# Performance work log

Hardware: AMD Instinct MI355X
Metric: run time of the kernel (lower is better)

Reference implementation:

```python
import jax, jax.numpy as jnp
import numpy as np

NUM_RAYS = 8192
NUM_POINTS = 1024
NEAR, FAR = 0.1, 6.0


def setup_inputs() -> dict:
    key = jax.random.key(0)
    k_rgb, k_alpha, k_jit, k_dir = jax.random.split(key, 4)
    raw_rgb_per_point = jax.random.uniform(k_rgb, (NUM_RAYS, NUM_POINTS, 3), dtype=jnp.float32)
    raw_alpha = jax.random.normal(k_alpha, (NUM_RAYS, NUM_POINTS), dtype=jnp.float32)
    # Monotonically increasing z values per ray (linspace + stratified jitter)
    t = jnp.linspace(0.0, 1.0, NUM_POINTS)[None, :]  # [1, P]
    jitter = jax.random.uniform(k_jit, (NUM_RAYS, NUM_POINTS), dtype=jnp.float32) / NUM_POINTS
    z_vals = (NEAR + (FAR - NEAR) * jnp.clip(t + jitter, 0.0, 1.0)).astype(jnp.float32)
    z_vals = jnp.sort(z_vals, axis=-1)
    rays_dir = jax.random.normal(k_dir, (NUM_RAYS, 3), dtype=jnp.float32)
    pruning_mask = jnp.ones((NUM_RAYS, NUM_POINTS), dtype=bool)
    return {
        "raw_rgb_per_point": raw_rgb_per_point,
        "raw_alpha": raw_alpha,
        "z_vals": z_vals,
        "rays_dir": rays_dir,
        "pruning_mask": pruning_mask,
        "points_per_ray": NUM_POINTS,
    }


def reference(raw_rgb_per_point, raw_alpha, z_vals, rays_dir, pruning_mask, points_per_ray):
    # Faithful eval-mode (is_training=False) translation of Renderer._compose_rays.
    corrective_factor = float(points_per_ray) / 1024.0
    FAR_DIST = 1e10

    # Distances between adjacent samples, last one padded to "infinity".
    dists = z_vals[..., 1:] - z_vals[..., :-1]                      # [R, P-1]
    dists = jnp.concatenate(
        [dists, jnp.full_like(dists[..., :1], FAR_DIST)], axis=-1)  # [R, P]
    dists = dists * jnp.linalg.norm(rays_dir, axis=-1, keepdims=True)

    # raw2alpha: 1 - exp(-relu(raw) * dist * cf)
    alpha = 1.0 - jnp.exp(-jax.nn.relu(raw_alpha) * dists * corrective_factor)  # [R, P]

    # Exclusive cumulative transmittance, then weights.
    trans = jnp.cumprod(
        jnp.concatenate([jnp.ones_like(alpha[:, :1]), 1.0 - alpha + 1e-10], axis=-1),
        axis=-1)[:, :-1]                                            # [R, P]
    weights = alpha * trans                                         # [R, P]

    rgb = jnp.einsum("rp,rpc->rc", weights, raw_rgb_per_point)      # [R, 3]
    accumulated_weights = jnp.sum(weights, axis=-1)                 # [R]

    depth = (jnp.sum(weights[:, :-1] * z_vals[:, :-1], axis=-1)
             + (1.0 - accumulated_weights + weights[:, -1]) * z_vals[:, -1])  # [R]

    disparity = 1.0 / jnp.maximum(1e-4, depth / accumulated_weights)          # [R]

    return rgb, accumulated_weights, depth, disparity
```

## Files before the change

kernel.cpp:

```cpp
#include <hip/hip_runtime.h>


#define NUM_RAYS 8192
#define P 1024
#define BLOCK 256
#define RAYS_PER_BLOCK 4

__global__ __launch_bounds__(256) void compose_rays_kernel(
    const float* __restrict__ rgb_in,
    const float* __restrict__ raw_alpha,
    const float* __restrict__ z_vals,
    const float* __restrict__ rays_dir,
    const int*   __restrict__ ppr,
    float* __restrict__ out)
{
    const int lane = threadIdx.x & 63;
    const int wid  = threadIdx.x >> 6;
    const int r    = blockIdx.x * RAYS_PER_BLOCK + wid;

    const float cf = (float)(*ppr) * (1.0f / 1024.0f);

    const float dx = rays_dir[r * 3 + 0];
    const float dy = rays_dir[r * 3 + 1];
    const float dz = rays_dir[r * 3 + 2];
    const float nrm = sqrtf(dx * dx + dy * dy + dz * dz);

    const size_t rowP = (size_t)r * P;

    float4 z4[4];
#pragma unroll
    for (int it = 0; it < 4; ++it)
        z4[it] = *(const float4*)(z_vals + rowP + it * 256 + lane * 4);

    float znext[4];
#pragma unroll
    for (int it = 0; it < 4; ++it) {
        const float from_next_lane = __shfl_down(z4[it].x, 1);
        const float first_of_next  = (it < 3) ? __shfl(z4[it + 1].x, 0) : 0.0f;
        znext[it] = (lane == 63) ? first_of_next : from_next_lane;
    }
    const float zl = __shfl(z4[3].w, 63);

    float carry = 1.0f;
    float ws = 0.f, rs = 0.f, gs = 0.f, bs = 0.f, ds = 0.f;
    float wlast = 0.f;

#pragma unroll
    for (int it = 0; it < 4; ++it) {
        const float4 a4 = *(const float4*)(raw_alpha + rowP + it * 256 + lane * 4);
        const float* rgbp = rgb_in + (size_t)r * (P * 3) + it * 768 + lane * 12;
        const float4 c0 = *(const float4*)(rgbp + 0);
        const float4 c1 = *(const float4*)(rgbp + 4);
        const float4 c2 = *(const float4*)(rgbp + 8);

        const float zv[4] = {z4[it].x, z4[it].y, z4[it].z, z4[it].w};
        const float av[4] = {a4.x, a4.y, a4.z, a4.w};
        float dists[4];
        dists[0] = (zv[1] - zv[0]) * nrm;
        dists[1] = (zv[2] - zv[1]) * nrm;
        dists[2] = (zv[3] - zv[2]) * nrm;
        dists[3] = ((it == 3 && lane == 63) ? 1e10f : (znext[it] - zv[3])) * nrm;

        float alpha[4], om[4];
        float local = 1.0f;
#pragma unroll
        for (int j = 0; j < 4; ++j) {
            const float ra = fmaxf(av[j], 0.0f);
            alpha[j] = 1.0f - expf(-ra * dists[j] * cf);
            om[j]    = 1.0f - alpha[j] + 1e-10f;
            local   *= om[j];
        }

        float v = local;
#pragma unroll
        for (int off = 1; off < 64; off <<= 1) {
            const float n = __shfl_up(v, off);
            if (lane >= off) v *= n;
        }
        const float total = __shfl(v, 63);
        float excl = __shfl_up(v, 1);
        if (lane == 0) excl = 1.0f;
        excl *= carry;
        carry *= total;

        const float rgbv[12] = {c0.x, c0.y, c0.z, c0.w, c1.x, c1.y, c1.z, c1.w,
                                c2.x, c2.y, c2.z, c2.w};
        float trun = excl;
#pragma unroll
        for (int j = 0; j < 4; ++j) {
            const float w = alpha[j] * trun;
            ws += w;
            rs += w * rgbv[3 * j + 0];
            gs += w * rgbv[3 * j + 1];
            bs += w * rgbv[3 * j + 2];
            if (it == 3 && lane == 63 && j == 3)
                wlast = w;
            else
                ds += w * zv[j];
            trun *= om[j];
        }
    }

    const float wl = __shfl(wlast, 63);

#pragma unroll
    for (int off = 32; off > 0; off >>= 1) {
        ws += __shfl_down(ws, off);
        rs += __shfl_down(rs, off);
        gs += __shfl_down(gs, off);
        bs += __shfl_down(bs, off);
        ds += __shfl_down(ds, off);
    }

    if (lane == 0) {
        const float depth = ds + (1.0f - ws + wl) * zl;
        const float disp  = 1.0f / fmaxf(1e-4f, depth / ws);
        out[r * 3 + 0] = rs;
        out[r * 3 + 1] = gs;
        out[r * 3 + 2] = bs;
        out[3 * NUM_RAYS + r] = ws;
        out[4 * NUM_RAYS + r] = depth;
        out[5 * NUM_RAYS + r] = disp;
    }
}

extern "C" void kernel_launch(void* const* d_in, const int* in_sizes, int n_in,
                              void* d_out, int out_size, void* d_ws, size_t ws_size,
                              hipStream_t stream) {
    const float* rgb_in    = (const float*)d_in[0];
    const float* raw_alpha = (const float*)d_in[1];
    const float* z_vals    = (const float*)d_in[2];
    const float* rays_dir  = (const float*)d_in[3];
    const int*   ppr       = (const int*)d_in[5];
    float* out = (float*)d_out;

    compose_rays_kernel<<<NUM_RAYS / RAYS_PER_BLOCK, BLOCK, 0, stream>>>(
        rgb_in, raw_alpha, z_vals, rays_dir, ppr, out);
}
```

Before: 31.25 us.

## Coalesce RGB loads and redistribute weights through LDS for colour accumulation

RGB loads change from a 48-byte per-lane stride to fully contiguous float4 loads across the wave. Each lane's four per-point weights are staged in shared memory so lanes can fetch the weights matching their interleaved RGB components. The block shrinks to two rays (128 threads). The change adds LDS traffic, a wait, and per-lane branching on the component phase in exchange for better load coalescing on the dominant RGB stream.

```diff
diff --git a/kernel.cpp b/kernel.cpp
--- a/kernel.cpp
+++ b/kernel.cpp
@@ -3,10 +3,10 @@
 
 #define NUM_RAYS 8192
 #define P 1024
-#define BLOCK 256
-#define RAYS_PER_BLOCK 4
+#define BLOCK 128
+#define RAYS_PER_BLOCK 2
 
-__global__ __launch_bounds__(256) void compose_rays_kernel(
+__global__ __launch_bounds__(128) void compose_rays_kernel(
     const float* __restrict__ rgb_in,
     const float* __restrict__ raw_alpha,
     const float* __restrict__ z_vals,
@@ -17,6 +17,8 @@
     const int lane = threadIdx.x & 63;
     const int wid  = threadIdx.x >> 6;
     const int r    = blockIdx.x * RAYS_PER_BLOCK + wid;
+
+    __shared__ float w_lds[RAYS_PER_BLOCK][4][256];
 
     const float cf = (float)(*ppr) * (1.0f / 1024.0f);
 
@@ -48,10 +50,10 @@
 #pragma unroll
     for (int it = 0; it < 4; ++it) {
         const float4 a4 = *(const float4*)(raw_alpha + rowP + it * 256 + lane * 4);
-        const float* rgbp = rgb_in + (size_t)r * (P * 3) + it * 768 + lane * 12;
-        const float4 c0 = *(const float4*)(rgbp + 0);
-        const float4 c1 = *(const float4*)(rgbp + 4);
-        const float4 c2 = *(const float4*)(rgbp + 8);
+        const float* cbase = rgb_in + (size_t)r * (P * 3) + it * 768;
+        const float4 c0 = *(const float4*)(cbase + 4 * (lane));
+        const float4 c1 = *(const float4*)(cbase + 4 * (lane + 64));
+        const float4 c2 = *(const float4*)(cbase + 4 * (lane + 128));
 
         const float zv[4] = {z4[it].x, z4[it].y, z4[it].z, z4[it].w};
         const float av[4] = {a4.x, a4.y, a4.z, a4.w};
@@ -83,21 +85,44 @@
         excl *= carry;
         carry *= total;
 
-        const float rgbv[12] = {c0.x, c0.y, c0.z, c0.w, c1.x, c1.y, c1.z, c1.w,
-                                c2.x, c2.y, c2.z, c2.w};
-        float trun = excl;
+        float4 wq;
+        {
+            float trun = excl;
+            float w0 = alpha[0] * trun; trun *= om[0];
+            float w1 = alpha[1] * trun; trun *= om[1];
+            float w2 = alpha[2] * trun; trun *= om[2];
+            float w3 = alpha[3] * trun;
+            wq = make_float4(w0, w1, w2, w3);
+            ws += w0 + w1 + w2 + w3;
+            ds += w0 * zv[0] + w1 * zv[1] + w2 * zv[2];
+            if (it == 3 && lane == 63)
+                wlast = w3;
+            else
+                ds += w3 * zv[3];
+        }
+
+        *(float4*)(&w_lds[wid][it][lane * 4]) = wq;
+        asm volatile("s_waitcnt lgkmcnt(0)" ::: "memory");
+
 #pragma unroll
-        for (int j = 0; j < 4; ++j) {
-            const float w = alpha[j] * trun;
-            ws += w;
-            rs += w * rgbv[3 * j + 0];
-            gs += w * rgbv[3 * j + 1];
-            bs += w * rgbv[3 * j + 2];
-            if (it == 3 && lane == 63 && j == 3)
-                wlast = w;
-            else
-                ds += w * zv[j];
-            trun *= om[j];
+        for (int k = 0; k < 3; ++k) {
+            const int   q  = lane + 64 * k;
+            const int   f  = 4 * q;
+            const int   p0 = f / 3;
+            const int   m3 = f - 3 * p0;
+            const float wA = w_lds[wid][it][p0];
+            const float wB = w_lds[wid][it][p0 + 1];
+            const float4 cv = (k == 0) ? c0 : (k == 1) ? c1 : c2;
+            if (m3 == 0) {
+                rs += cv.x * wA; gs += cv.y * wA; bs += cv.z * wA;
+                rs += cv.w * wB;
+            } else if (m3 == 1) {
+                gs += cv.x * wA; bs += cv.y * wA;
+                rs += cv.z * wB; gs += cv.w * wB;
+            } else {
+                bs += cv.x * wA;
+                rs += cv.y * wB; gs += cv.z * wB; bs += cv.w * wB;
+            }
         }
     }
 
```

Result: no change. 30.74 us (-1.6%).
